# Optimization experiments

Measured on AMD Instinct MI355X. Metric: run time of the kernel, lower is better.

## Reference

```python
import jax, jax.numpy as jnp
import numpy as np

N_NODES = 100000
N_EDGES = 3200000
IN_DIM, H_DIM, OUT_DIM = 512, 256, 128
NEG_SLOPE = 0.25


def setup_inputs() -> dict:
    key = jax.random.key(0)
    ks = jax.random.split(key, 8)
    x = jax.random.normal(ks[0], (N_NODES, IN_DIM), dtype=jnp.float32)
    # xavier-normal-ish init for weights, zero bias (matches module init)
    W1 = jax.random.normal(ks[1], (IN_DIM, H_DIM), dtype=jnp.float32) * np.sqrt(2.0 / (IN_DIM + H_DIM))
    b1 = jnp.zeros((H_DIM,), dtype=jnp.float32)
    W2 = jax.random.normal(ks[2], (H_DIM, OUT_DIM), dtype=jnp.float32) * np.sqrt(2.0 / (H_DIM + OUT_DIM))
    b2 = jnp.zeros((OUT_DIM,), dtype=jnp.float32)
    adj_row = jax.random.randint(ks[3], (N_EDGES,), 0, N_NODES, dtype=jnp.int32)
    adj_col = jax.random.randint(ks[4], (N_EDGES,), 0, N_NODES, dtype=jnp.int32)
    # positive normalized-ish edge weights (like D^-1/2 A D^-1/2 entries)
    edge_weight = jax.random.uniform(ks[5], (N_EDGES,), dtype=jnp.float32) * 0.05
    return {"x": x, "W1": W1, "b1": b1, "W2": W2, "b2": b2,
            "adj_row": adj_row, "adj_col": adj_col, "edge_weight": edge_weight}


def reference(x, W1, b1, W2, b2, adj_row, adj_col, edge_weight):
    n = x.shape[0]

    def spmm(support):
        # out[r] = sum over edges (r, c): w * support[c]   (COO SpMM)
        msgs = edge_weight[:, None] * support[adj_col]  # [E, d] gather
        return jax.ops.segment_sum(msgs, adj_row, num_segments=n)

    def leaky(h):
        return jnp.where(h > 0, h, NEG_SLOPE * h)

    h = leaky(spmm(x @ W1) + b1)          # gc1 + leaky_relu (dropout = eval mode)
    h = leaky(spmm(h @ W2) + b2)          # gc2 + leaky_relu
    return h
```

## Files before the change

kernel.cpp:

```cpp
#include <hip/hip_runtime.h>

typedef unsigned short u16;
typedef unsigned char u8;
typedef __attribute__((ext_vector_type(8))) __bf16 bf16x8;
typedef __attribute__((ext_vector_type(4))) float f32x4;

#define CAP   4608
#define CAPO  5504
#define CHUNK 8192
#define NBKT_PAD 800
#define NBAND 32

static __device__ __forceinline__ u16 f2bf(float f) {
    return __builtin_bit_cast(u16, (__bf16)f);
}
static __device__ __forceinline__ void gl_lds16(const void* g, void* l) {
    __builtin_amdgcn_global_load_lds((const __attribute__((address_space(1))) void*)g,
                                     (__attribute__((address_space(3))) void*)l, 16, 0, 0);
}


__global__ __launch_bounds__(256) void bucket_k(const int* __restrict__ row,
                                                const int* __restrict__ col,
                                                const float* __restrict__ w,
                                                int* __restrict__ gcount,
                                                int2* __restrict__ edges, int E) {
    __shared__ int hist[NBKT_PAD];
    __shared__ int lscan[NBKT_PAD];
    __shared__ int lcnt[NBKT_PAD];
    __shared__ int gbase[NBKT_PAD];
    __shared__ int tsum[256];
    __shared__ int2 pay[CHUNK];
    __shared__ int  dst[CHUNK];
    const int base = blockIdx.x * CHUNK;
    const int cntC = min(CHUNK, E - base);
    const int tid = threadIdx.x;

    for (int i = tid; i < NBKT_PAD; i += 256) { hist[i] = 0; lcnt[i] = 0; }
    __syncthreads();

    for (int i = tid; i < cntC; i += 256) atomicAdd(&hist[row[base + i] >> 7], 1);
    __syncthreads();

    int h[4], s = 0;
    #pragma unroll
    for (int j = 0; j < 4; ++j) {
        int bb = tid * 4 + j;
        h[j] = (bb < NBKT_PAD) ? hist[bb] : 0;
        s += h[j];
    }
    tsum[tid] = s;
    __syncthreads();
    for (int d = 1; d < 256; d <<= 1) {
        int t = (tid >= d) ? tsum[tid - d] : 0;
        __syncthreads();
        tsum[tid] += t;
        __syncthreads();
    }
    int run = tsum[tid] - s;
    #pragma unroll
    for (int j = 0; j < 4; ++j) {
        int bb = tid * 4 + j;
        if (bb < NBKT_PAD) {
            lscan[bb] = run;
            run += h[j];
            if (h[j] > 0) gbase[bb] = atomicAdd(&gcount[bb], h[j]);
        }
    }
    __syncthreads();

    for (int i = tid; i < cntC; i += 256) {
        int r = row[base + i];
        int c = col[base + i];
        float ww = w[base + i];
        int bb = r >> 7;
        int lp = atomicAdd(&lcnt[bb], 1);
        int slot = lscan[bb] + lp;
        int pos = gbase[bb] + lp;
        pay[slot] = make_int2(((r & 127) << 17) | c, __float_as_int(ww));
        dst[slot] = (pos < CAP) ? bb * CAP + pos : -1;
    }
    __syncthreads();

    for (int i = tid; i < cntC; i += 256) {
        int d = dst[i];
        if (d >= 0) edges[d] = pay[i];
    }
}


__global__ __launch_bounds__(256) void rsort_k(const int* __restrict__ gcount,
                                               const int2* __restrict__ edges,
                                               int* __restrict__ colsO,
                                               float* __restrict__ wO,
                                               int2* __restrict__ rc, int n) {
    __shared__ int cnt2[128 * NBAND];
    __shared__ int base2[128 * NBAND];
    __shared__ int colsL[CAPO];
    __shared__ float wL[CAPO];
    __shared__ int sc[128];
    const int b = blockIdx.x, tid = threadIdx.x;
    const int cnt = min(gcount[b], CAP);
    const int2* eb = edges + (size_t)b * CAP;

    for (int i = tid; i < 128 * NBAND; i += 256) cnt2[i] = 0;
    for (int i = tid; i < CAPO; i += 256) { colsL[i] = 0; wL[i] = 0.f; }
    __syncthreads();

    for (int i = tid; i < cnt; i += 256) {
        int2 e = eb[i];
        int rr = ((unsigned)e.x) >> 17;
        int cc = e.x & 0x1FFFF;
        atomicAdd(&cnt2[rr * NBAND + (cc >> 12)], 1);
    }
    __syncthreads();

    int rtot = 0;
    if (tid < 128) {
        #pragma unroll
        for (int bb = 0; bb < NBAND; ++bb) rtot += cnt2[tid * NBAND + bb];
        rtot = (rtot + 7) & ~7;
        sc[tid] = rtot;
    }
    __syncthreads();
    for (int d = 1; d < 128; d <<= 1) {
        int t = 0;
        if (tid < 128 && tid >= d) t = sc[tid - d];
        __syncthreads();
        if (tid < 128) sc[tid] += t;
        __syncthreads();
    }
    if (tid < 128) {
        int start = sc[tid] - rtot;
        int gr = b * 128 + tid;
        if (gr < n) rc[gr] = make_int2(b * CAPO + start, rtot);
        int run = start;
        #pragma unroll
        for (int bb = 0; bb < NBAND; ++bb) {
            base2[tid * NBAND + bb] = run;
            run += cnt2[tid * NBAND + bb];
        }
    }
    __syncthreads();

    for (int i = tid; i < cnt; i += 256) {
        int2 e = eb[i];
        int rr = ((unsigned)e.x) >> 17;
        int cc = e.x & 0x1FFFF;
        int slot = atomicAdd(&base2[rr * NBAND + (cc >> 12)], 1);
        colsL[slot] = cc << 8;
        wL[slot] = __int_as_float(e.y);
    }
    __syncthreads();

    int* co = colsO + (size_t)b * CAPO;
    float* wo = wO + (size_t)b * CAPO;
    for (int i = tid; i < CAPO; i += 256) { co[i] = colsL[i]; wo[i] = wL[i]; }
}


__global__ __launch_bounds__(256) void wscale_k(const int* __restrict__ cols,
                                                const float* __restrict__ wr,
                                                const float* __restrict__ scales,
                                                float* __restrict__ ws, int total) {
    int i = (blockIdx.x * 256 + threadIdx.x) * 4;
    const int stride = gridDim.x * 1024;
    for (; i < total; i += stride) {
        int4 c = *(const int4*)(cols + i);
        float4 w = *(const float4*)(wr + i);
        float4 o;
        o.x = w.x * scales[((unsigned)c.x) >> 8];
        o.y = w.y * scales[((unsigned)c.y) >> 8];
        o.z = w.z * scales[((unsigned)c.z) >> 8];
        o.w = w.w * scales[((unsigned)c.w) >> 8];
        *(float4*)(ws + i) = o;
    }
}


__global__ void transpose_w2(const float* __restrict__ W1, u16* __restrict__ W1T,
                             const float* __restrict__ W2, u16* __restrict__ W2T,
                             int* __restrict__ gcount) {
    const int T1 = 512 * 256;
    const int T2 = 256 * 128;
    int i = blockIdx.x * blockDim.x + threadIdx.x;
    if (i < NBKT_PAD) gcount[i] = 0;
    if (i < T1) {
        int k = i / 256, nn = i % 256;
        W1T[nn * 512 + k] = f2bf(W1[i]);
    } else if (i < T1 + T2) {
        int j = i - T1;
        int k = j / 128, nn = j % 128;
        W2T[nn * 256 + k] = f2bf(W2[j]);
    }
}


template <int K, int NWN, bool AF32>
__global__ void gemm_fq(const void* __restrict__ Ap,
                        const u16* __restrict__ BT,
                        u8* __restrict__ supq,
                        float* __restrict__ scales, int M) {
    constexpr int BN = NWN * 64;
    constexpr int THREADS = NWN * 128;
    constexpr int A_ISS = 8192 / (THREADS * 16);
    constexpr int B_ISS = (BN * 64) / (THREADS * 16);
    constexpr int LOGN = (NWN == 4) ? 2 : 1;
    static_assert(!AF32 || (4096 / (THREADS * 8)) == 1, "AF32 path assumes A_CH==1");
    __shared__ alignas(16) u16 As[128 * 32];
    __shared__ alignas(16) u16 Bs[BN * 32];
    __shared__ float rmax[128][NWN];
    __shared__ u8 qtile[128 * BN];

    const int tid = threadIdx.x;
    const int lane = tid & 63, wv = tid >> 6;
    const int wm = wv >> LOGN, wn = wv & (NWN - 1);
    const int lr = lane & 15, lg = lane >> 4;
    const int mblk = blockIdx.x;
    f32x4 acc[4][4] = {};
    const float* Af = (const float*)Ap;
    const u16* Ab = (const u16*)Ap;

    const u16* gB[B_ISS];
    u16* lB[B_ISS];
    #pragma unroll
    for (int i = 0; i < B_ISS; ++i) {
        int t8 = i * THREADS + tid;
        gB[i] = BT + (long)(t8 >> 2) * K + (t8 & 3) * 8;
        lB[i] = Bs + i * THREADS * 8 + wv * 512;
    }

    if constexpr (AF32) {
        long r = (long)mblk * 128 + (tid >> 2);
        if (r >= M) r = M - 1;
        const float* gAf0 = Af + r * K + (tid & 3) * 8;
        u16* lAf0 = As + (tid >> 2) * 32 + (tid & 3) * 8;

        float4 pf0 = *(const float4*)(gAf0 + 0);
        float4 pf1 = *(const float4*)(gAf0 + 4);
        #pragma unroll 4
        for (int kt = 0; kt < K; kt += 32) {
            #pragma unroll
            for (int i = 0; i < B_ISS; ++i) gl_lds16(gB[i] + kt, lB[i]);
            __builtin_amdgcn_sched_barrier(0);
            const int ktn = (kt + 32 < K) ? kt + 32 : 0;
            float4 nf0 = *(const float4*)(gAf0 + ktn);
            float4 nf1 = *(const float4*)(gAf0 + ktn + 4);
            bf16x8 t;
            t[0] = (__bf16)pf0.x; t[1] = (__bf16)pf0.y; t[2] = (__bf16)pf0.z; t[3] = (__bf16)pf0.w;
            t[4] = (__bf16)pf1.x; t[5] = (__bf16)pf1.y; t[6] = (__bf16)pf1.z; t[7] = (__bf16)pf1.w;
            *(bf16x8*)lAf0 = t;
            asm volatile("s_waitcnt vmcnt(2) lgkmcnt(0)" ::: "memory");
            __builtin_amdgcn_sched_barrier(0);
            __builtin_amdgcn_s_barrier();
            __builtin_amdgcn_sched_barrier(0);

            bf16x8 a[4], b[4];
            #pragma unroll
            for (int mi = 0; mi < 4; ++mi)
                a[mi] = *(const bf16x8*)&As[(wm * 64 + mi * 16 + lr) * 32 + lg * 8];
            #pragma unroll
            for (int ni = 0; ni < 4; ++ni)
                b[ni] = *(const bf16x8*)&Bs[(wn * 64 + ni * 16 + lr) * 32 + lg * 8];
            #pragma unroll
            for (int mi = 0; mi < 4; ++mi)
                #pragma unroll
                for (int ni = 0; ni < 4; ++ni)
                    acc[mi][ni] = __builtin_amdgcn_mfma_f32_16x16x32_bf16(a[mi], b[ni], acc[mi][ni], 0, 0, 0);
            __builtin_amdgcn_sched_barrier(0);
            __builtin_amdgcn_s_barrier();
            __builtin_amdgcn_sched_barrier(0);
            pf0 = nf0; pf1 = nf1;
        }
    } else {
        const u16* gA[A_ISS];
        u16* lA[A_ISS];
        #pragma unroll
        for (int i = 0; i < A_ISS; ++i) {
            int t8 = i * THREADS + tid;
            long r = (long)mblk * 128 + (t8 >> 2);
            if (r >= M) r = M - 1;
            gA[i] = Ab + r * K + (t8 & 3) * 8;
            lA[i] = As + i * THREADS * 8 + wv * 512;
        }
        #pragma unroll 2
        for (int kt = 0; kt < K; kt += 32) {
            #pragma unroll
            for (int i = 0; i < A_ISS; ++i) gl_lds16(gA[i] + kt, lA[i]);
            #pragma unroll
            for (int i = 0; i < B_ISS; ++i) gl_lds16(gB[i] + kt, lB[i]);
            __syncthreads();

            bf16x8 a[4], b[4];
            #pragma unroll
            for (int mi = 0; mi < 4; ++mi)
                a[mi] = *(const bf16x8*)&As[(wm * 64 + mi * 16 + lr) * 32 + lg * 8];
            #pragma unroll
            for (int ni = 0; ni < 4; ++ni)
                b[ni] = *(const bf16x8*)&Bs[(wn * 64 + ni * 16 + lr) * 32 + lg * 8];
            #pragma unroll
            for (int mi = 0; mi < 4; ++mi)
                #pragma unroll
                for (int ni = 0; ni < 4; ++ni)
                    acc[mi][ni] = __builtin_amdgcn_mfma_f32_16x16x32_bf16(a[mi], b[ni], acc[mi][ni], 0, 0, 0);
            __syncthreads();
        }
    }

    #pragma unroll
    for (int mi = 0; mi < 4; ++mi) {
        #pragma unroll
        for (int j = 0; j < 4; ++j) {
            float m = 0.f;
            #pragma unroll
            for (int ni = 0; ni < 4; ++ni) m = fmaxf(m, fabsf(acc[mi][ni][j]));
            m = fmaxf(m, __shfl_xor(m, 1));
            m = fmaxf(m, __shfl_xor(m, 2));
            m = fmaxf(m, __shfl_xor(m, 4));
            m = fmaxf(m, __shfl_xor(m, 8));
            if (lr == 0) rmax[wm * 64 + mi * 16 + lg * 4 + j][wn] = m;
        }
    }
    __syncthreads();

    #pragma unroll
    for (int mi = 0; mi < 4; ++mi) {
        #pragma unroll
        for (int j = 0; j < 4; ++j) {
            const int rl = wm * 64 + mi * 16 + lg * 4 + j;
            float m = rmax[rl][0];
            #pragma unroll
            for (int w2 = 1; w2 < NWN; ++w2) m = fmaxf(m, rmax[rl][w2]);
            const float inv = (m > 0.f) ? 127.f / m : 0.f;
            #pragma unroll
            for (int ni = 0; ni < 4; ++ni) {
                int q = (int)rintf(acc[mi][ni][j] * inv) + 128;
                qtile[rl * BN + wn * 64 + ni * 16 + lr] = (u8)q;
            }
        }
    }
    if (tid < 128) {
        int gr = mblk * 128 + tid;
        if (gr < M) {
            float m = rmax[tid][0];
            #pragma unroll
            for (int w2 = 1; w2 < NWN; ++w2) m = fmaxf(m, rmax[tid][w2]);
            scales[gr] = m * (1.f / 127.f);
        }
    }
    __syncthreads();

    constexpr int CHUNKS = (128 * BN) / (THREADS * 16);
    #pragma unroll
    for (int cc = 0; cc < CHUNKS; ++cc) {
        int off = cc * THREADS * 16 + tid * 16;
        int gr = mblk * 128 + off / BN;
        if (gr < M)
            *(int4*)(supq + (size_t)mblk * 128 * BN + off) = *(const int4*)&qtile[off];
    }
}


__global__ __launch_bounds__(256) void spmm_l1(const int2* __restrict__ rc,
                                               const int* __restrict__ cols,
                                               const float* __restrict__ ws,
                                               const u8* __restrict__ supq,
                                               const float* __restrict__ bias,
                                               u16* __restrict__ obf, int n) {
    const int r = blockIdx.x * 4 + (threadIdx.x >> 6);
    if (r >= n) return;
    const int lane = threadIdx.x & 63;
    const int half = lane >> 5;
    const unsigned lsub8 = (unsigned)(lane & 31) * 8;
    float acc[8] = {0.f, 0.f, 0.f, 0.f, 0.f, 0.f, 0.f, 0.f};
    float kk = 0.f;
    const int2 se = rc[r];
    const int e0  = __builtin_amdgcn_readfirstlane(se.x);
    const int cnt = __builtin_amdgcn_readfirstlane(se.y);
    const int* __restrict__ cp = cols + e0;
    const float* __restrict__ wp = ws + e0;

#define L1_LOAD(CA, CB, WA, WB, G0, G1, G2, G3, IDX)                                   \
    CA = *(const int4*)(cp + (IDX));   CB = *(const int4*)(cp + (IDX) + 4);            \
    WA = *(const float4*)(wp + (IDX)); WB = *(const float4*)(wp + (IDX) + 4);          \
    G0 = *(const uint2*)(supq + (((unsigned)(half ? CA.y : CA.x)) + lsub8));           \
    G1 = *(const uint2*)(supq + (((unsigned)(half ? CA.w : CA.z)) + lsub8));           \
    G2 = *(const uint2*)(supq + (((unsigned)(half ? CB.y : CB.x)) + lsub8));           \
    G3 = *(const uint2*)(supq + (((unsigned)(half ? CB.w : CB.z)) + lsub8));

#define L1_PAIR(WX, WY, G)                                                              \
    {   const float wsel = half ? (WY) : (WX);                                          \
        kk += wsel;                                                                     \
        acc[0] += wsel * (float)((G).x & 0xFF);                                         \
        acc[1] += wsel * (float)(((G).x >> 8) & 0xFF);                                  \
        acc[2] += wsel * (float)(((G).x >> 16) & 0xFF);                                 \
        acc[3] += wsel * (float)((G).x >> 24);                                          \
        acc[4] += wsel * (float)((G).y & 0xFF);                                         \
        acc[5] += wsel * (float)(((G).y >> 8) & 0xFF);                                  \
        acc[6] += wsel * (float)(((G).y >> 16) & 0xFF);                                 \
        acc[7] += wsel * (float)((G).y >> 24); }

#define L1_CONS(WA, WB, G0, G1, G2, G3)                                                 \
    L1_PAIR(WA.x, WA.y, G0) L1_PAIR(WA.z, WA.w, G1)                                     \
    L1_PAIR(WB.x, WB.y, G2) L1_PAIR(WB.z, WB.w, G3)

    if (cnt > 0) {
        int4 ca0, cb0; float4 wa0, wb0; uint2 g0, g1, g2, g3;
        L1_LOAD(ca0, cb0, wa0, wb0, g0, g1, g2, g3, 0)
        int i = 8;
        while (i < cnt) {
            int4 ca1, cb1; float4 wa1, wb1; uint2 h0, h1, h2, h3;
            L1_LOAD(ca1, cb1, wa1, wb1, h0, h1, h2, h3, i)
            L1_CONS(wa0, wb0, g0, g1, g2, g3)
            wa0 = wa1; wb0 = wb1; g0 = h0; g1 = h1; g2 = h2; g3 = h3;
            i += 8;
        }
        L1_CONS(wa0, wb0, g0, g1, g2, g3)
    }
#undef L1_LOAD
#undef L1_PAIR
#undef L1_CONS

    kk += __shfl_xor(kk, 32);
    #pragma unroll
    for (int j = 0; j < 8; ++j) acc[j] += __shfl_xor(acc[j], 32);

    const float off = 128.f * kk;
    float a0 = half ? acc[4] : acc[0];
    float a1 = half ? acc[5] : acc[1];
    float a2 = half ? acc[6] : acc[2];
    float a3 = half ? acc[7] : acc[3];
    const int d0 = (lane & 31) * 8 + half * 4;
    const float4 bb = *(const float4*)&bias[d0];
    float h0 = a0 - off + bb.x, h1 = a1 - off + bb.y;
    float h2 = a2 - off + bb.z, h3 = a3 - off + bb.w;
    h0 = h0 > 0.f ? h0 : 0.25f * h0;
    h1 = h1 > 0.f ? h1 : 0.25f * h1;
    h2 = h2 > 0.f ? h2 : 0.25f * h2;
    h3 = h3 > 0.f ? h3 : 0.25f * h3;
    ushort4 hv; hv.x = f2bf(h0); hv.y = f2bf(h1); hv.z = f2bf(h2); hv.w = f2bf(h3);
    *(ushort4*)&obf[(size_t)r * 256 + d0] = hv;
}


__global__ __launch_bounds__(256) void spmm_l2(const int2* __restrict__ rc,
                                               const int* __restrict__ cols,
                                               const float* __restrict__ ws,
                                               const u8* __restrict__ supq,
                                               const float* __restrict__ bias,
                                               float* __restrict__ of32, int n) {
    const int r = blockIdx.x * 4 + (threadIdx.x >> 6);
    if (r >= n) return;
    const int lane = threadIdx.x & 63;
    const int quad = lane >> 4;
    const unsigned lsub8 = (unsigned)(lane & 15) * 8;
    float acc[8] = {0.f, 0.f, 0.f, 0.f, 0.f, 0.f, 0.f, 0.f};
    float kk = 0.f;
    const int2 se = rc[r];
    const int e0  = __builtin_amdgcn_readfirstlane(se.x);
    const int cnt = __builtin_amdgcn_readfirstlane(se.y);
    const int* __restrict__ cp = cols + e0;
    const float* __restrict__ wp = ws + e0;

#define L2_SELI(CA) ((quad & 2) ? ((quad & 1) ? (CA).w : (CA).z) : ((quad & 1) ? (CA).y : (CA).x))
#define L2_SELF(WA) ((quad & 2) ? ((quad & 1) ? (WA).w : (WA).z) : ((quad & 1) ? (WA).y : (WA).x))

#define L2_LOAD(CA, CB, WA, WB, G0, G1, IDX)                                           \
    CA = *(const int4*)(cp + (IDX));   CB = *(const int4*)(cp + (IDX) + 4);            \
    WA = *(const float4*)(wp + (IDX)); WB = *(const float4*)(wp + (IDX) + 4);          \
    G0 = *(const uint2*)(supq + ((((unsigned)L2_SELI(CA)) >> 1) + lsub8));             \
    G1 = *(const uint2*)(supq + ((((unsigned)L2_SELI(CB)) >> 1) + lsub8));

#define L2_QUAD(WA, G)                                                                  \
    {   const float wsel = L2_SELF(WA);                                                 \
        kk += wsel;                                                                     \
        acc[0] += wsel * (float)((G).x & 0xFF);                                         \
        acc[1] += wsel * (float)(((G).x >> 8) & 0xFF);                                  \
        acc[2] += wsel * (float)(((G).x >> 16) & 0xFF);                                 \
        acc[3] += wsel * (float)((G).x >> 24);                                          \
        acc[4] += wsel * (float)((G).y & 0xFF);                                         \
        acc[5] += wsel * (float)(((G).y >> 8) & 0xFF);                                  \
        acc[6] += wsel * (float)(((G).y >> 16) & 0xFF);                                 \
        acc[7] += wsel * (float)((G).y >> 24); }

    if (cnt > 0) {
        int4 ca0, cb0; float4 wa0, wb0; uint2 g0, g1;
        L2_LOAD(ca0, cb0, wa0, wb0, g0, g1, 0)
        int i = 8;
        while (i < cnt) {
            int4 ca1, cb1; float4 wa1, wb1; uint2 h0, h1;
            L2_LOAD(ca1, cb1, wa1, wb1, h0, h1, i)
            L2_QUAD(wa0, g0) L2_QUAD(wb0, g1)
            wa0 = wa1; wb0 = wb1; g0 = h0; g1 = h1;
            i += 8;
        }
        L2_QUAD(wa0, g0) L2_QUAD(wb0, g1)
    }
#undef L2_LOAD
#undef L2_QUAD
#undef L2_SELI
#undef L2_SELF

    kk += __shfl_xor(kk, 16);
    kk += __shfl_xor(kk, 32);
    #pragma unroll
    for (int j = 0; j < 8; ++j) {
        acc[j] += __shfl_xor(acc[j], 16);
        acc[j] += __shfl_xor(acc[j], 32);
    }

    const float off = 128.f * kk;
    float a0 = (quad & 2) ? ((quad & 1) ? acc[6] : acc[4]) : ((quad & 1) ? acc[2] : acc[0]);
    float a1 = (quad & 2) ? ((quad & 1) ? acc[7] : acc[5]) : ((quad & 1) ? acc[3] : acc[1]);
    const int d0 = (lane & 15) * 8 + quad * 2;
    const float2 bb = *(const float2*)&bias[d0];
    float h0 = a0 - off + bb.x, h1 = a1 - off + bb.y;
    h0 = h0 > 0.f ? h0 : 0.25f * h0;
    h1 = h1 > 0.f ? h1 : 0.25f * h1;
    *(float2*)&of32[(size_t)r * 128 + d0] = make_float2(h0, h1);
}


extern "C" void kernel_launch(void* const* d_in, const int* in_sizes, int n_in,
                              void* d_out, int out_size, void* d_ws, size_t ws_size,
                              hipStream_t stream) {
    const float* x  = (const float*)d_in[0];
    const float* W1 = (const float*)d_in[1];
    const float* b1 = (const float*)d_in[2];
    const float* W2 = (const float*)d_in[3];
    const float* b2 = (const float*)d_in[4];
    const int* arow = (const int*)d_in[5];
    const int* acol = (const int*)d_in[6];
    const float* ew = (const float*)d_in[7];

    const int IN = 512, H = 256, OUT = 128;
    const int n = in_sizes[0] / IN;
    const int E = in_sizes[5];
    const int nbkt = (n + 127) >> 7;
    const int totS = nbkt * CAPO;

    char* base = (char*)d_ws;
    size_t off = 0;
    auto carve = [&](size_t bytes) -> void* {
        void* r = base + off;
        off = (off + bytes + 255) & ~(size_t)255;
        return r;
    };
    int*   gcount = (int*)carve((size_t)NBKT_PAD * 4);
    int2*  edges  = (int2*)carve((size_t)nbkt * CAP * 8);
    int*   colsS  = (int*)carve((size_t)totS * 4);
    float* wraw   = (float*)carve((size_t)totS * 4);
    float* wsS    = (float*)carve((size_t)totS * 4);
    int2*  rc     = (int2*)carve((size_t)n * 8);
    u16*   W1T    = (u16*)carve((size_t)H * IN * 2);
    u16*   W2T    = (u16*)carve((size_t)OUT * H * 2);
    u8*    supq   = (u8*)carve((size_t)n * H);
    float* scales = (float*)carve((size_t)n * 4);
    u16*   h1     = (u16*)carve((size_t)n * H * 2);

    transpose_w2<<<(512 * 256 + 256 * 128 + 255) / 256, 256, 0, stream>>>(W1, W1T, W2, W2T, gcount);

    bucket_k<<<(E + CHUNK - 1) / CHUNK, 256, 0, stream>>>(arow, acol, ew, gcount, edges, E);
    rsort_k<<<nbkt, 256, 0, stream>>>(gcount, edges, colsS, wraw, rc, n);

    gemm_fq<512, 4, true><<<(n + 127) / 128, 512, 0, stream>>>(x, W1T, supq, scales, n);
    wscale_k<<<(totS / 4 + 255) / 256, 256, 0, stream>>>(colsS, wraw, scales, wsS, totS);
    spmm_l1<<<(n + 3) / 4, 256, 0, stream>>>(rc, colsS, wsS, supq, b1, h1, n);

    gemm_fq<256, 2, false><<<(n + 127) / 128, 256, 0, stream>>>(h1, W2T, supq, scales, n);
    wscale_k<<<(totS / 4 + 255) / 256, 256, 0, stream>>>(colsS, wraw, scales, wsS, totS);
    spmm_l2<<<(n + 3) / 4, 256, 0, stream>>>(rc, colsS, wsS, supq, b2, (float*)d_out, n);
}
```

Baseline: 437.5 us.

## Deepen SpMM gather prefetch to four stages and drop column banding in row sort

Both SpMM kernels now keep four groups of 8-edge gathers in flight, a rotating software pipeline, where before there was a single-stage prefetch. The goal is to hide the latency of random gathers. Edge weights are now loaded at consume time instead of being prefetched. The row sort no longer bands edges by column within each row; it uses a plain per-row histogram, which makes the sort cheaper but loses the column locality of the gathers. A 64-entry zeroed tail is added to the edge arrays so the speculative loads stay in bounds.

```diff
diff --git a/kernel.cpp b/kernel.cpp
--- a/kernel.cpp
+++ b/kernel.cpp
@@ -9,7 +9,6 @@
 #define CAPO  5504
 #define CHUNK 8192
 #define NBKT_PAD 800
-#define NBAND 32
 
 static __device__ __forceinline__ u16 f2bf(float f) {
     return __builtin_bit_cast(u16, (__bf16)f);
@@ -93,35 +92,26 @@
                                                const int2* __restrict__ edges,
                                                int* __restrict__ colsO,
                                                float* __restrict__ wO,
-                                               int2* __restrict__ rc, int n) {
-    __shared__ int cnt2[128 * NBAND];
-    __shared__ int base2[128 * NBAND];
+                                               int2* __restrict__ rc, int n, int nbkt) {
+    __shared__ int hist[128];
+    __shared__ int sbase[128];
+    __shared__ int lcnt[128];
+    __shared__ int sc[128];
     __shared__ int colsL[CAPO];
     __shared__ float wL[CAPO];
-    __shared__ int sc[128];
     const int b = blockIdx.x, tid = threadIdx.x;
     const int cnt = min(gcount[b], CAP);
     const int2* eb = edges + (size_t)b * CAP;
 
-    for (int i = tid; i < 128 * NBAND; i += 256) cnt2[i] = 0;
+    if (tid < 128) { hist[tid] = 0; lcnt[tid] = 0; }
     for (int i = tid; i < CAPO; i += 256) { colsL[i] = 0; wL[i] = 0.f; }
     __syncthreads();
 
-    for (int i = tid; i < cnt; i += 256) {
-        int2 e = eb[i];
-        int rr = ((unsigned)e.x) >> 17;
-        int cc = e.x & 0x1FFFF;
-        atomicAdd(&cnt2[rr * NBAND + (cc >> 12)], 1);
-    }
-    __syncthreads();
-
-    int rtot = 0;
-    if (tid < 128) {
-        #pragma unroll
-        for (int bb = 0; bb < NBAND; ++bb) rtot += cnt2[tid * NBAND + bb];
-        rtot = (rtot + 7) & ~7;
-        sc[tid] = rtot;
-    }
+    for (int i = tid; i < cnt; i += 256) atomicAdd(&hist[((unsigned)eb[i].x) >> 17], 1);
+    __syncthreads();
+
+    int hp = 0;
+    if (tid < 128) { hp = (hist[tid] + 7) & ~7; sc[tid] = hp; }
     __syncthreads();
     for (int d = 1; d < 128; d <<= 1) {
         int t = 0;
@@ -131,24 +121,18 @@
         __syncthreads();
     }
     if (tid < 128) {
-        int start = sc[tid] - rtot;
+        int start = sc[tid] - hp;
+        sbase[tid] = start;
         int gr = b * 128 + tid;
-        if (gr < n) rc[gr] = make_int2(b * CAPO + start, rtot);
-        int run = start;
-        #pragma unroll
-        for (int bb = 0; bb < NBAND; ++bb) {
-            base2[tid * NBAND + bb] = run;
-            run += cnt2[tid * NBAND + bb];
-        }
+        if (gr < n) rc[gr] = make_int2(b * CAPO + start, hp);
     }
     __syncthreads();
 
     for (int i = tid; i < cnt; i += 256) {
         int2 e = eb[i];
         int rr = ((unsigned)e.x) >> 17;
-        int cc = e.x & 0x1FFFF;
-        int slot = atomicAdd(&base2[rr * NBAND + (cc >> 12)], 1);
-        colsL[slot] = cc << 8;
+        int slot = sbase[rr] + atomicAdd(&lcnt[rr], 1);
+        colsL[slot] = (e.x & 0x1FFFF) << 8;
         wL[slot] = __int_as_float(e.y);
     }
     __syncthreads();
@@ -156,6 +140,10 @@
     int* co = colsO + (size_t)b * CAPO;
     float* wo = wO + (size_t)b * CAPO;
     for (int i = tid; i < CAPO; i += 256) { co[i] = colsL[i]; wo[i] = wL[i]; }
+    if (b == nbkt - 1 && tid < 64) {
+        colsO[(size_t)nbkt * CAPO + tid] = 0;
+        wO[(size_t)nbkt * CAPO + tid] = 0.f;
+    }
 }
 
 
@@ -380,46 +368,58 @@
     const int* __restrict__ cp = cols + e0;
     const float* __restrict__ wp = ws + e0;
 
-#define L1_LOAD(CA, CB, WA, WB, G0, G1, G2, G3, IDX)                                   \
-    CA = *(const int4*)(cp + (IDX));   CB = *(const int4*)(cp + (IDX) + 4);            \
-    WA = *(const float4*)(wp + (IDX)); WB = *(const float4*)(wp + (IDX) + 4);          \
-    G0 = *(const uint2*)(supq + (((unsigned)(half ? CA.y : CA.x)) + lsub8));           \
-    G1 = *(const uint2*)(supq + (((unsigned)(half ? CA.w : CA.z)) + lsub8));           \
-    G2 = *(const uint2*)(supq + (((unsigned)(half ? CB.y : CB.x)) + lsub8));           \
-    G3 = *(const uint2*)(supq + (((unsigned)(half ? CB.w : CB.z)) + lsub8));
-
-#define L1_PAIR(WX, WY, G)                                                              \
-    {   const float wsel = half ? (WY) : (WX);                                          \
-        kk += wsel;                                                                     \
-        acc[0] += wsel * (float)((G).x & 0xFF);                                         \
-        acc[1] += wsel * (float)(((G).x >> 8) & 0xFF);                                  \
-        acc[2] += wsel * (float)(((G).x >> 16) & 0xFF);                                 \
-        acc[3] += wsel * (float)((G).x >> 24);                                          \
-        acc[4] += wsel * (float)((G).y & 0xFF);                                         \
-        acc[5] += wsel * (float)(((G).y >> 8) & 0xFF);                                  \
-        acc[6] += wsel * (float)(((G).y >> 16) & 0xFF);                                 \
-        acc[7] += wsel * (float)((G).y >> 24); }
-
-#define L1_CONS(WA, WB, G0, G1, G2, G3)                                                 \
-    L1_PAIR(WA.x, WA.y, G0) L1_PAIR(WA.z, WA.w, G1)                                     \
-    L1_PAIR(WB.x, WB.y, G2) L1_PAIR(WB.z, WB.w, G3)
+#define L1_ISSUE(G0, G1, G2, G3, IDX) {                                              \
+    int4 ca = *(const int4*)(cp + (IDX));                                            \
+    int4 cb = *(const int4*)(cp + (IDX) + 4);                                        \
+    G0 = *(const uint2*)(supq + ((unsigned)(half ? ca.y : ca.x) + lsub8));           \
+    G1 = *(const uint2*)(supq + ((unsigned)(half ? ca.w : ca.z) + lsub8));           \
+    G2 = *(const uint2*)(supq + ((unsigned)(half ? cb.y : cb.x) + lsub8));           \
+    G3 = *(const uint2*)(supq + ((unsigned)(half ? cb.w : cb.z) + lsub8)); }
+
+#define L1_PAIR(WX, WY, G) {                                                         \
+    const float wsel = half ? (WY) : (WX);                                           \
+    kk += wsel;                                                                      \
+    acc[0] += wsel * (float)((G).x & 0xFF);                                          \
+    acc[1] += wsel * (float)(((G).x >> 8) & 0xFF);                                   \
+    acc[2] += wsel * (float)(((G).x >> 16) & 0xFF);                                  \
+    acc[3] += wsel * (float)((G).x >> 24);                                           \
+    acc[4] += wsel * (float)((G).y & 0xFF);                                          \
+    acc[5] += wsel * (float)(((G).y >> 8) & 0xFF);                                   \
+    acc[6] += wsel * (float)(((G).y >> 16) & 0xFF);                                  \
+    acc[7] += wsel * (float)((G).y >> 24); }
+
+#define L1_CONSUME(G0, G1, G2, G3, IDX) {                                            \
+    float4 wa = *(const float4*)(wp + (IDX));                                        \
+    float4 wb = *(const float4*)(wp + (IDX) + 4);                                    \
+    L1_PAIR(wa.x, wa.y, G0) L1_PAIR(wa.z, wa.w, G1)                                  \
+    L1_PAIR(wb.x, wb.y, G2) L1_PAIR(wb.z, wb.w, G3) }
 
     if (cnt > 0) {
-        int4 ca0, cb0; float4 wa0, wb0; uint2 g0, g1, g2, g3;
-        L1_LOAD(ca0, cb0, wa0, wb0, g0, g1, g2, g3, 0)
-        int i = 8;
-        while (i < cnt) {
-            int4 ca1, cb1; float4 wa1, wb1; uint2 h0, h1, h2, h3;
-            L1_LOAD(ca1, cb1, wa1, wb1, h0, h1, h2, h3, i)
-            L1_CONS(wa0, wb0, g0, g1, g2, g3)
-            wa0 = wa1; wb0 = wb1; g0 = h0; g1 = h1; g2 = h2; g3 = h3;
-            i += 8;
-        }
-        L1_CONS(wa0, wb0, g0, g1, g2, g3)
-    }
-#undef L1_LOAD
+        uint2 a0, a1, a2, a3, b0, b1, b2, b3, c0, c1, c2, c3, d0, d1, d2, d3;
+        L1_ISSUE(a0, a1, a2, a3, 0)
+        if (8 < cnt)  L1_ISSUE(b0, b1, b2, b3, 8)
+        if (16 < cnt) L1_ISSUE(c0, c1, c2, c3, 16)
+        if (24 < cnt) L1_ISSUE(d0, d1, d2, d3, 24)
+        int i = 0;
+        while (i + 32 < cnt) {
+            L1_CONSUME(a0, a1, a2, a3, i)
+            L1_ISSUE(a0, a1, a2, a3, i + 32)
+            L1_CONSUME(b0, b1, b2, b3, i + 8)
+            if (i + 40 < cnt) L1_ISSUE(b0, b1, b2, b3, i + 40)
+            L1_CONSUME(c0, c1, c2, c3, i + 16)
+            if (i + 48 < cnt) L1_ISSUE(c0, c1, c2, c3, i + 48)
+            L1_CONSUME(d0, d1, d2, d3, i + 24)
+            if (i + 56 < cnt) L1_ISSUE(d0, d1, d2, d3, i + 56)
+            i += 32;
+        }
+        if (i < cnt)      L1_CONSUME(a0, a1, a2, a3, i)
+        if (i + 8 < cnt)  L1_CONSUME(b0, b1, b2, b3, i + 8)
+        if (i + 16 < cnt) L1_CONSUME(c0, c1, c2, c3, i + 16)
+        if (i + 24 < cnt) L1_CONSUME(d0, d1, d2, d3, i + 24)
+    }
+#undef L1_ISSUE
 #undef L1_PAIR
-#undef L1_CONS
+#undef L1_CONSUME
 
     kk += __shfl_xor(kk, 32);
     #pragma unroll
@@ -465,39 +465,56 @@
 #define L2_SELI(CA) ((quad & 2) ? ((quad & 1) ? (CA).w : (CA).z) : ((quad & 1) ? (CA).y : (CA).x))
 #define L2_SELF(WA) ((quad & 2) ? ((quad & 1) ? (WA).w : (WA).z) : ((quad & 1) ? (WA).y : (WA).x))
 
-#define L2_LOAD(CA, CB, WA, WB, G0, G1, IDX)                                           \
-    CA = *(const int4*)(cp + (IDX));   CB = *(const int4*)(cp + (IDX) + 4);            \
-    WA = *(const float4*)(wp + (IDX)); WB = *(const float4*)(wp + (IDX) + 4);          \
-    G0 = *(const uint2*)(supq + ((((unsigned)L2_SELI(CA)) >> 1) + lsub8));             \
-    G1 = *(const uint2*)(supq + ((((unsigned)L2_SELI(CB)) >> 1) + lsub8));
-
-#define L2_QUAD(WA, G)                                                                  \
-    {   const float wsel = L2_SELF(WA);                                                 \
-        kk += wsel;                                                                     \
-        acc[0] += wsel * (float)((G).x & 0xFF);                                         \
-        acc[1] += wsel * (float)(((G).x >> 8) & 0xFF);                                  \
-        acc[2] += wsel * (float)(((G).x >> 16) & 0xFF);                                 \
-        acc[3] += wsel * (float)((G).x >> 24);                                          \
-        acc[4] += wsel * (float)((G).y & 0xFF);                                         \
-        acc[5] += wsel * (float)(((G).y >> 8) & 0xFF);                                  \
-        acc[6] += wsel * (float)(((G).y >> 16) & 0xFF);                                 \
-        acc[7] += wsel * (float)((G).y >> 24); }
+#define L2_ISSUE(G0, G1, IDX) {                                                      \
+    int4 ca = *(const int4*)(cp + (IDX));                                            \
+    int4 cb = *(const int4*)(cp + (IDX) + 4);                                        \
+    G0 = *(const uint2*)(supq + ((((unsigned)L2_SELI(ca)) >> 1) + lsub8));           \
+    G1 = *(const uint2*)(supq + ((((unsigned)L2_SELI(cb)) >> 1) + lsub8)); }
+
+#define L2_QUAD(WSEL, G) {                                                           \
+    kk += WSEL;                                                                      \
+    acc[0] += WSEL * (float)((G).x & 0xFF);                                          \
+    acc[1] += WSEL * (float)(((G).x >> 8) & 0xFF);                                   \
+    acc[2] += WSEL * (float)(((G).x >> 16) & 0xFF);                                  \
+    acc[3] += WSEL * (float)((G).x >> 24);                                           \
+    acc[4] += WSEL * (float)((G).y & 0xFF);                                          \
+    acc[5] += WSEL * (float)(((G).y >> 8) & 0xFF);                                   \
+    acc[6] += WSEL * (float)(((G).y >> 16) & 0xFF);                                  \
+    acc[7] += WSEL * (float)((G).y >> 24); }
+
+#define L2_CONSUME(G0, G1, IDX) {                                                    \
+    float4 wa = *(const float4*)(wp + (IDX));                                        \
+    float4 wb = *(const float4*)(wp + (IDX) + 4);                                    \
+    const float wsa = L2_SELF(wa);                                                   \
+    const float wsb = L2_SELF(wb);                                                   \
+    L2_QUAD(wsa, G0) L2_QUAD(wsb, G1) }
 
     if (cnt > 0) {
-        int4 ca0, cb0; float4 wa0, wb0; uint2 g0, g1;
-        L2_LOAD(ca0, cb0, wa0, wb0, g0, g1, 0)
-        int i = 8;
-        while (i < cnt) {
-            int4 ca1, cb1; float4 wa1, wb1; uint2 h0, h1;
-            L2_LOAD(ca1, cb1, wa1, wb1, h0, h1, i)
-            L2_QUAD(wa0, g0) L2_QUAD(wb0, g1)
-            wa0 = wa1; wb0 = wb1; g0 = h0; g1 = h1;
-            i += 8;
-        }
-        L2_QUAD(wa0, g0) L2_QUAD(wb0, g1)
-    }
-#undef L2_LOAD
+        uint2 a0, a1, b0, b1, c0, c1, d0, d1;
+        L2_ISSUE(a0, a1, 0)
+        if (8 < cnt)  L2_ISSUE(b0, b1, 8)
+        if (16 < cnt) L2_ISSUE(c0, c1, 16)
+        if (24 < cnt) L2_ISSUE(d0, d1, 24)
+        int i = 0;
+        while (i + 32 < cnt) {
+            L2_CONSUME(a0, a1, i)
+            L2_ISSUE(a0, a1, i + 32)
+            L2_CONSUME(b0, b1, i + 8)
+            if (i + 40 < cnt) L2_ISSUE(b0, b1, i + 40)
+            L2_CONSUME(c0, c1, i + 16)
+            if (i + 48 < cnt) L2_ISSUE(c0, c1, i + 48)
+            L2_CONSUME(d0, d1, i + 24)
+            if (i + 56 < cnt) L2_ISSUE(d0, d1, i + 56)
+            i += 32;
+        }
+        if (i < cnt)      L2_CONSUME(a0, a1, i)
+        if (i + 8 < cnt)  L2_CONSUME(b0, b1, i + 8)
+        if (i + 16 < cnt) L2_CONSUME(c0, c1, i + 16)
+        if (i + 24 < cnt) L2_CONSUME(d0, d1, i + 24)
+    }
+#undef L2_ISSUE
 #undef L2_QUAD
+#undef L2_CONSUME
 #undef L2_SELI
 #undef L2_SELF
 
@@ -538,6 +555,7 @@
     const int E = in_sizes[5];
     const int nbkt = (n + 127) >> 7;
     const int totS = nbkt * CAPO;
+    const int totS2 = totS + 64;
 
     char* base = (char*)d_ws;
     size_t off = 0;
@@ -548,9 +566,9 @@
     };
     int*   gcount = (int*)carve((size_t)NBKT_PAD * 4);
     int2*  edges  = (int2*)carve((size_t)nbkt * CAP * 8);
-    int*   colsS  = (int*)carve((size_t)totS * 4);
-    float* wraw   = (float*)carve((size_t)totS * 4);
-    float* wsS    = (float*)carve((size_t)totS * 4);
+    int*   colsS  = (int*)carve((size_t)totS2 * 4);
+    float* wraw   = (float*)carve((size_t)totS2 * 4);
+    float* wsS    = (float*)carve((size_t)totS2 * 4);
     int2*  rc     = (int2*)carve((size_t)n * 8);
     u16*   W1T    = (u16*)carve((size_t)H * IN * 2);
     u16*   W2T    = (u16*)carve((size_t)OUT * H * 2);
@@ -561,13 +579,13 @@
     transpose_w2<<<(512 * 256 + 256 * 128 + 255) / 256, 256, 0, stream>>>(W1, W1T, W2, W2T, gcount);
 
     bucket_k<<<(E + CHUNK - 1) / CHUNK, 256, 0, stream>>>(arow, acol, ew, gcount, edges, E);
-    rsort_k<<<nbkt, 256, 0, stream>>>(gcount, edges, colsS, wraw, rc, n);
+    rsort_k<<<nbkt, 256, 0, stream>>>(gcount, edges, colsS, wraw, rc, n, nbkt);
 
     gemm_fq<512, 4, true><<<(n + 127) / 128, 512, 0, stream>>>(x, W1T, supq, scales, n);
-    wscale_k<<<(totS / 4 + 255) / 256, 256, 0, stream>>>(colsS, wraw, scales, wsS, totS);
+    wscale_k<<<(totS2 / 4 + 255) / 256, 256, 0, stream>>>(colsS, wraw, scales, wsS, totS2);
     spmm_l1<<<(n + 3) / 4, 256, 0, stream>>>(rc, colsS, wsS, supq, b1, h1, n);
 
     gemm_fq<256, 2, false><<<(n + 127) / 128, 256, 0, stream>>>(h1, W2T, supq, scales, n);
-    wscale_k<<<(totS / 4 + 255) / 256, 256, 0, stream>>>(colsS, wraw, scales, wsS, totS);
+    wscale_k<<<(totS2 / 4 + 255) / 256, 256, 0, stream>>>(colsS, wraw, scales, wsS, totS2);
     spmm_l2<<<(n + 3) / 4, 256, 0, stream>>>(rc, colsS, wsS, supq, b2, (float*)d_out, n);
 }
```

New measurement: 470.6 us. 1.08x slower.
